# Kernel tuning notes

Measured on AMD Instinct MI355X. Metric: run time of the kernel, lower is better.

The kernel has to match this reference:

```python
import jax, jax.numpy as jnp
import numpy as np

N_NODES = 100000
N_EDGES = 1200000
D = 64
BN_EPS = 1e-5


def setup_inputs() -> dict:
    key = jax.random.key(0)
    ks = jax.random.split(key, 6)
    x = jax.random.normal(ks[0], (N_NODES, D), dtype=jnp.float32)
    edge_index = jax.random.randint(ks[1], (2, N_EDGES), 0, N_NODES, dtype=jnp.int64)
    # Linear params (Kaiming-uniform style scale)
    lim = 1.0 / np.sqrt(D)
    W = jax.random.uniform(ks[2], (D, D), dtype=jnp.float32, minval=-lim, maxval=lim)
    b = jax.random.uniform(ks[3], (D,), dtype=jnp.float32, minval=-lim, maxval=lim)
    gamma = jnp.ones((D,), dtype=jnp.float32)
    beta = jnp.zeros((D,), dtype=jnp.float32)
    C = jax.random.normal(ks[4], (D, D), dtype=jnp.float32) * 0.1
    return {"x": x, "edge_index": edge_index, "W": W, "b": b,
            "gamma": gamma, "beta": beta, "C": C}


def reference(x, edge_index, W, b, gamma, beta, C):
    n = x.shape[0]
    src, dst = edge_index[0], edge_index[1]
    # SimpleConv(aggr='mean', combine_root='sum'): mean over incoming messages + root
    msg_sum = jax.ops.segment_sum(x[src], dst, num_segments=n)            # [N, D]
    deg = jax.ops.segment_sum(jnp.ones_like(src, dtype=x.dtype), dst, num_segments=n)
    agg = msg_sum / jnp.maximum(deg, 1.0)[:, None]
    h = x + agg
    # Linear
    h = h @ W.T + b
    # BatchNorm1d (training mode: batch stats, biased variance)
    mean = jnp.mean(h, axis=0)
    var = jnp.mean((h - mean) ** 2, axis=0)
    h = (h - mean) * jax.lax.rsqrt(var + BN_EPS) * gamma + beta
    # AsymSwiGLU gate
    gate = jax.nn.sigmoid(h @ C)
    return gate * h
```

## Files before the change

kernel.cpp:

```cpp
#include <hip/hip_runtime.h>
#include <math.h>

#define D 64
#define BN_EPS 1e-5f

#define NBITS 7
#define BINSZ 128
#define MAXBINS 800
#define CAP 2048
#define CHUNK 4096
#define BUCKET 48
#define OP 68
#define WP 72

typedef short bf16x8 __attribute__((ext_vector_type(8)));
typedef float f32x4 __attribute__((ext_vector_type(4)));

__device__ __forceinline__ unsigned f2bf(float f) {
    unsigned u = __float_as_uint(f);
    return (u + 0x7FFFu + ((u >> 16) & 1u)) >> 16;
}
__device__ __forceinline__ float bf2f(unsigned short h) {
    return __uint_as_float(((unsigned)h) << 16);
}
__device__ __forceinline__ bf16x8 cvt8f(const float* __restrict__ p) {
    float4 a = ((const float4*)p)[0];
    float4 b = ((const float4*)p)[1];
    bf16x8 r;
    r[0] = (short)f2bf(a.x); r[1] = (short)f2bf(a.y);
    r[2] = (short)f2bf(a.z); r[3] = (short)f2bf(a.w);
    r[4] = (short)f2bf(b.x); r[5] = (short)f2bf(b.y);
    r[6] = (short)f2bf(b.z); r[7] = (short)f2bf(b.w);
    return r;
}

__global__ __launch_bounds__(256) void zero_kernel(int4* __restrict__ p, int n4) {
    int t = blockIdx.x * 256 + threadIdx.x;
    if (t < n4) p[t] = make_int4(0, 0, 0, 0);
}

__global__ __launch_bounds__(256) void xhalf_kernel(
    const float* __restrict__ x, unsigned short* __restrict__ xh, long long n8) {
    long long t = (long long)blockIdx.x * 256 + threadIdx.x;
    if (t >= n8) return;
    const float4* rp = (const float4*)(x + t * 8);
    float4 a = rp[0], b = rp[1];
    uint4 o;
    o.x = f2bf(a.x) | (f2bf(a.y) << 16);
    o.y = f2bf(a.z) | (f2bf(a.w) << 16);
    o.z = f2bf(b.x) | (f2bf(b.y) << 16);
    o.w = f2bf(b.z) | (f2bf(b.w) << 16);
    *(uint4*)(xh + t * 8) = o;
}

__global__ __launch_bounds__(1024) void binA_kernel(
    const int* __restrict__ ei, int* __restrict__ binCursor,
    unsigned* __restrict__ binBuf, int E, int nbins) {
    __shared__ unsigned short pos[CHUNK];
    __shared__ int hist[MAXBINS];
    __shared__ int base[MAXBINS];
    int tid = threadIdx.x;
    int c0 = blockIdx.x * CHUNK;

    for (int i = tid; i < nbins; i += 1024) hist[i] = 0;
    __syncthreads();

#pragma unroll
    for (int k = 0; k < CHUNK / 1024; ++k) {
        int i = k * 1024 + tid;
        int e = c0 + i;
        if (e < E) {
            int dst = ei[E + e];
            pos[i] = (unsigned short)atomicAdd(&hist[dst >> NBITS], 1);
        }
    }
    __syncthreads();

    for (int b = tid; b < nbins; b += 1024) {
        int h = hist[b];
        base[b] = h > 0 ? atomicAdd(&binCursor[b * 16], h) : 0;
    }
    __syncthreads();

#pragma unroll
    for (int k = 0; k < CHUNK / 1024; ++k) {
        int i = k * 1024 + tid;
        int e = c0 + i;
        if (e < E) {
            int src = ei[e];
            int dst = ei[E + e];
            int b = dst >> NBITS;
            int idx = base[b] + (int)pos[i];
            if (idx < CAP)
                binBuf[(size_t)b * CAP + idx] =
                    ((unsigned)src << NBITS) | (unsigned)(dst & (BINSZ - 1));
        }
    }
}

__global__ __launch_bounds__(256) void binSort_kernel(
    const unsigned* __restrict__ binBuf, const int* __restrict__ binCursor,
    int* __restrict__ csr, int* __restrict__ cnt, int N) {
    __shared__ int hist[BINSZ];
    int bin = blockIdx.x, tid = threadIdx.x;
    int nodeBase = bin << NBITS;
    int nrows = N - nodeBase; if (nrows > BINSZ) nrows = BINSZ;
    if (tid < BINSZ) hist[tid] = 0;
    __syncthreads();
    int nE = binCursor[bin * 16]; if (nE > CAP) nE = CAP;
    const unsigned* eb = binBuf + (size_t)bin * CAP;
    for (int i = tid; i < nE; i += 256) {
        unsigned r = eb[i];
        int dl = (int)(r & (BINSZ - 1));
        int src = (int)(r >> NBITS);
        int p = atomicAdd(&hist[dl], 1);
        if (p < BUCKET) csr[(size_t)(nodeBase + dl) * BUCKET + p] = src;
    }
    __syncthreads();
    for (int r = tid; r < nrows; r += 256) cnt[nodeBase + r] = hist[r];
}

__global__ __launch_bounds__(1024) void fusedGL_kernel(
    const unsigned short* __restrict__ xh, const int* __restrict__ csr,
    const int* __restrict__ cnt, const float* __restrict__ W,
    const float* __restrict__ bias, float* __restrict__ h,
    float* __restrict__ partial, int N) {
    __shared__ float tile[64 * OP];
    __shared__ unsigned short wt[64 * WP];
    __shared__ float psum[16 * 32];
    int tid = threadIdx.x;
    int lane = tid & 63;
    int w = tid >> 6;
    int rbase = blockIdx.x << 6;
    int nrows = N - rbase; if (nrows > 64) nrows = 64;

    {
        int r = tid >> 4, q = tid & 15;
        float4 v = *(const float4*)(W + (size_t)r * D + q * 4);
        uint2 o;
        o.x = f2bf(v.x) | (f2bf(v.y) << 16);
        o.y = f2bf(v.z) | (f2bf(v.w) << 16);
        *(uint2*)(wt + r * WP + q * 4) = o;
    }

    int c = lane & 15, g = lane >> 4;
    for (int i = 0; i < 4; ++i) {
        int nl = w * 4 + i;
        int node = rbase + nl;
        if (node < N) {
            int deg = cnt[node];
            deg = __builtin_amdgcn_readfirstlane(deg);
            int trips = deg < BUCKET ? deg : BUCKET;
            int sidx = lane < BUCKET ? csr[(size_t)node * BUCKET + lane] : 0;
            float a0 = 0.f, a1 = 0.f, a2 = 0.f, a3 = 0.f;
            if (trips > 0) {
                int nq = (trips + 3) >> 2;
                int last = trips - 1;
                uint2 v[12];
#pragma unroll
                for (int q = 0; q < 12; ++q) {
                    if (q < nq) {
                        int r = 4 * q + g;
                        int rc = r < trips ? r : last;
                        int s = __shfl(sidx, rc);
                        v[q] = *(const uint2*)(xh + (size_t)s * D + c * 4);
                    }
                }
#pragma unroll
                for (int q = 0; q < 12; ++q) {
                    if (q < nq) {
                        int r = 4 * q + g;
                        if (r < trips) {
                            unsigned lo = v[q].x, hi = v[q].y;
                            a0 += __uint_as_float(lo << 16);
                            a1 += __uint_as_float(lo & 0xFFFF0000u);
                            a2 += __uint_as_float(hi << 16);
                            a3 += __uint_as_float(hi & 0xFFFF0000u);
                        }
                    }
                }
            }
            a0 += __shfl_xor(a0, 16); a0 += __shfl_xor(a0, 32);
            a1 += __shfl_xor(a1, 16); a1 += __shfl_xor(a1, 32);
            a2 += __shfl_xor(a2, 16); a2 += __shfl_xor(a2, 32);
            a3 += __shfl_xor(a3, 16); a3 += __shfl_xor(a3, 32);
            float invd = deg > 0 ? 1.0f / (float)deg : 1.0f;
            if (g == 0) {
                uint2 rt = *(const uint2*)(xh + (size_t)node * D + c * 4);
                float4 o;
                o.x = __uint_as_float(rt.x << 16)         + a0 * invd;
                o.y = __uint_as_float(rt.x & 0xFFFF0000u) + a1 * invd;
                o.z = __uint_as_float(rt.y << 16)         + a2 * invd;
                o.w = __uint_as_float(rt.y & 0xFFFF0000u) + a3 * invd;
                *(float4*)(tile + nl * OP + c * 4) = o;
            }
        } else {
            if (g == 0)
                *(float4*)(tile + nl * OP + c * 4) = make_float4(0.f, 0.f, 0.f, 0.f);
        }
    }
    __syncthreads();

    int rb = w & 3, t = w >> 2;
    int ar = lane & 15, gg = lane >> 4;
    const float* arow = tile + (rb * 16 + ar) * OP + 8 * gg;
    bf16x8 A0 = cvt8f(arow);
    bf16x8 A1 = cvt8f(arow + 32);
    bf16x8 B0 = *(const bf16x8*)(wt + (t * 16 + ar) * WP + 8 * gg);
    bf16x8 B1 = *(const bf16x8*)(wt + (t * 16 + ar) * WP + 32 + 8 * gg);
    float bj = bias[t * 16 + ar];
    f32x4 acc;
    acc[0] = bj; acc[1] = bj; acc[2] = bj; acc[3] = bj;
    acc = __builtin_amdgcn_mfma_f32_16x16x32_bf16(A0, B0, acc, 0, 0, 0);
    acc = __builtin_amdgcn_mfma_f32_16x16x32_bf16(A1, B1, acc, 0, 0, 0);
    __syncthreads();

#pragma unroll
    for (int r = 0; r < 4; ++r)
        tile[(rb * 16 + 4 * gg + r) * OP + t * 16 + ar] = acc[r];
    float s = 0.f, q = 0.f;
#pragma unroll
    for (int r = 0; r < 4; ++r) {
        int row = rb * 16 + 4 * gg + r;
        float v = (row < nrows) ? acc[r] : 0.f;
        s += v; q += v * v;
    }
    s += __shfl_xor(s, 16); s += __shfl_xor(s, 32);
    q += __shfl_xor(q, 16); q += __shfl_xor(q, 32);
    if (lane < 16) {
        psum[w * 32 + lane] = s;
        psum[w * 32 + 16 + lane] = q;
    }
    __syncthreads();

    {
        int r = tid >> 4, cq = tid & 15;
        if (r < nrows)
            *(float4*)(h + (size_t)(rbase + r) * D + cq * 4) =
                *(const float4*)(tile + r * OP + cq * 4);
    }
    if (tid < 128) {
        int f = tid & 63;
        int off = (tid >= 64) ? 16 : 0;
        int t2 = f >> 4, col = f & 15;
        float a = 0.f;
#pragma unroll
        for (int rb2 = 0; rb2 < 4; ++rb2)
            a += psum[(t2 * 4 + rb2) * 32 + off + col];
        partial[(size_t)blockIdx.x * 128 + tid] = a;
    }
}

__global__ __launch_bounds__(256) void reduceBN_kernel(
    const float* __restrict__ partial, const float* __restrict__ gamma,
    const float* __restrict__ beta, float* __restrict__ ss,
    int nWG, float inv_n) {
    __shared__ float rs[256], rq[256];
    int f = blockIdx.x;
    int tid = threadIdx.x;
    float s = 0.f, q = 0.f;
    for (int w = tid; w < nWG; w += 256) {
        s += partial[(size_t)w * 128 + f];
        q += partial[(size_t)w * 128 + 64 + f];
    }
    rs[tid] = s; rq[tid] = q;
    __syncthreads();
    for (int st = 128; st > 0; st >>= 1) {
        if (tid < st) { rs[tid] += rs[tid + st]; rq[tid] += rq[tid + st]; }
        __syncthreads();
    }
    if (tid == 0) {
        float mean = rs[0] * inv_n;
        float var = rq[0] * inv_n - mean * mean;
        float rstd = rsqrtf(var + BN_EPS);
        float sc = gamma[f] * rstd;
        ss[f] = sc;
        ss[64 + f] = beta[f] - mean * sc;
    }
}

__global__ __launch_bounds__(256) void gateMFMA_kernel(
    float* __restrict__ h, const float* __restrict__ ss,
    const float* __restrict__ C, int N) {
    __shared__ float tile[64 * OP];
    __shared__ unsigned short ct[64 * WP];
    int tid = threadIdx.x;
    int lane = tid & 63;
    int w = tid >> 6;
    int ar = lane & 15, g = lane >> 4;
    int rbase = blockIdx.x << 6;
    int nrows = N - rbase; if (nrows > 64) nrows = 64;

#pragma unroll
    for (int it = 0; it < 4; ++it) {
        int u = it * 256 + tid;
        int r = u >> 4, c = u & 15;
        float4 v = (r < nrows)
            ? *(const float4*)(h + (size_t)(rbase + r) * D + c * 4)
            : make_float4(0.f, 0.f, 0.f, 0.f);
        *(float4*)(tile + r * OP + c * 4) = v;
    }
    {
        int k = tid >> 2, q = tid & 3;
        const float* cp = C + (size_t)k * D + q * 16;
#pragma unroll
        for (int i = 0; i < 16; ++i)
            ct[(q * 16 + i) * WP + k] = (unsigned short)f2bf(cp[i]);
    }
    __syncthreads();

    bool valid = (rbase + w * 16) < N;
    f32x4 acc[4];
    if (valid) {
        const float* arow = tile + (w * 16 + ar) * OP + 8 * g;
        float4 s0 = *(const float4*)(ss + 8 * g);
        float4 s1 = *(const float4*)(ss + 8 * g + 4);
        float4 o0 = *(const float4*)(ss + 64 + 8 * g);
        float4 o1 = *(const float4*)(ss + 64 + 8 * g + 4);
        float4 v0 = ((const float4*)arow)[0];
        float4 v1 = ((const float4*)arow)[1];
        bf16x8 a0, a1;
        a0[0] = (short)f2bf(v0.x * s0.x + o0.x);
        a0[1] = (short)f2bf(v0.y * s0.y + o0.y);
        a0[2] = (short)f2bf(v0.z * s0.z + o0.z);
        a0[3] = (short)f2bf(v0.w * s0.w + o0.w);
        a0[4] = (short)f2bf(v1.x * s1.x + o1.x);
        a0[5] = (short)f2bf(v1.y * s1.y + o1.y);
        a0[6] = (short)f2bf(v1.z * s1.z + o1.z);
        a0[7] = (short)f2bf(v1.w * s1.w + o1.w);
        float4 t0 = *(const float4*)(ss + 32 + 8 * g);
        float4 t1 = *(const float4*)(ss + 32 + 8 * g + 4);
        float4 u0 = *(const float4*)(ss + 96 + 8 * g);
        float4 u1 = *(const float4*)(ss + 96 + 8 * g + 4);
        float4 w0 = ((const float4*)(arow + 32))[0];
        float4 w1 = ((const float4*)(arow + 32))[1];
        a1[0] = (short)f2bf(w0.x * t0.x + u0.x);
        a1[1] = (short)f2bf(w0.y * t0.y + u0.y);
        a1[2] = (short)f2bf(w0.z * t0.z + u0.z);
        a1[3] = (short)f2bf(w0.w * t0.w + u0.w);
        a1[4] = (short)f2bf(w1.x * t1.x + u1.x);
        a1[5] = (short)f2bf(w1.y * t1.y + u1.y);
        a1[6] = (short)f2bf(w1.z * t1.z + u1.z);
        a1[7] = (short)f2bf(w1.w * t1.w + u1.w);
#pragma unroll
        for (int t = 0; t < 4; ++t) {
            bf16x8 b0 = *(const bf16x8*)(ct + (t * 16 + ar) * WP + 8 * g);
            bf16x8 b1 = *(const bf16x8*)(ct + (t * 16 + ar) * WP + 32 + 8 * g);
            acc[t][0] = 0.f; acc[t][1] = 0.f; acc[t][2] = 0.f; acc[t][3] = 0.f;
            acc[t] = __builtin_amdgcn_mfma_f32_16x16x32_bf16(a0, b0, acc[t], 0, 0, 0);
            acc[t] = __builtin_amdgcn_mfma_f32_16x16x32_bf16(a1, b1, acc[t], 0, 0, 0);
        }
#pragma unroll
        for (int t = 0; t < 4; ++t) {
            float scC = ss[t * 16 + ar];
            float shC = ss[64 + t * 16 + ar];
#pragma unroll
            for (int r = 0; r < 4; ++r) {
                int idx = (w * 16 + 4 * g + r) * OP + t * 16 + ar;
                float hn = tile[idx] * scC + shC;
                float gg = 1.0f / (1.0f + __expf(-acc[t][r]));
                tile[idx] = gg * hn;
            }
        }
    }
    __syncthreads();

#pragma unroll
    for (int it = 0; it < 4; ++it) {
        int u = it * 256 + tid;
        int r = u >> 4, c = u & 15;
        if (r < nrows)
            *(float4*)(h + (size_t)(rbase + r) * D + c * 4) =
                *(const float4*)(tile + r * OP + c * 4);
    }
}

extern "C" void kernel_launch(void* const* d_in, const int* in_sizes, int n_in,
                              void* d_out, int out_size, void* d_ws, size_t ws_size,
                              hipStream_t stream) {
    const float* x     = (const float*)d_in[0];
    const int*   ei    = (const int*)d_in[1];
    const float* W     = (const float*)d_in[2];
    const float* b     = (const float*)d_in[3];
    const float* gamma = (const float*)d_in[4];
    const float* beta  = (const float*)d_in[5];
    const float* C     = (const float*)d_in[6];
    float* out = (float*)d_out;

    const int N = in_sizes[0] / D;
    const int E = in_sizes[1] / 2;
    const int nbins = (N + BINSZ - 1) >> NBITS;
    const int nWGlin = (N + 63) / 64;

    int*            binCursor = (int*)d_ws;
    float*          ss        = (float*)(binCursor + (size_t)nbins * 16);
    int*            cnt       = (int*)(ss + 128);
    int*            csr       = cnt + N;
    unsigned*       binBuf    = (unsigned*)(csr + (size_t)N * BUCKET);
    float*          partial   = (float*)(binBuf + (size_t)nbins * CAP);
    unsigned short* xh        = (unsigned short*)(partial + (size_t)nWGlin * 128);

    {
        int n4 = (nbins * 16 + 128) / 4;
        zero_kernel<<<(n4 + 255) / 256, 256, 0, stream>>>((int4*)d_ws, n4);
    }
    {
        long long n8 = (long long)N * D / 8;
        xhalf_kernel<<<(int)((n8 + 255) / 256), 256, 0, stream>>>(x, xh, n8);
    }
    binA_kernel<<<(E + CHUNK - 1) / CHUNK, 1024, 0, stream>>>(ei, binCursor, binBuf, E, nbins);
    binSort_kernel<<<nbins, 256, 0, stream>>>(binBuf, binCursor, csr, cnt, N);
    fusedGL_kernel<<<nWGlin, 1024, 0, stream>>>(xh, csr, cnt, W, b, out, partial, N);
    reduceBN_kernel<<<64, 256, 0, stream>>>(partial, gamma, beta, ss, nWGlin, 1.0f / (float)N);
    gateMFMA_kernel<<<(N + 63) / 64, 256, 0, stream>>>(out, ss, C, N);
}
```

Before: 117.4 us.

## Fuse bin sort into gather-linear kernel with LDS-resident per-node CSR

Removes the separate binSort kernel and its global CSR and count arrays. Each gather-linear workgroup now scans its half of a 128-node bin from binBuf and builds a 64-node bucketed adjacency list and degree histogram in shared memory, aliased onto the output tile buffer. This drops a kernel launch and a large global write and read of the padded CSR, at the cost of every bin being scanned twice, once by each half-workgroup. It also writes the aggregated tile directly as bf16 into a separate LDS buffer, which removes the fp32-to-bf16 conversion at the MFMA operand load and one barrier.

```diff
diff --git a/kernel.cpp b/kernel.cpp
--- a/kernel.cpp
+++ b/kernel.cpp
@@ -22,16 +22,6 @@
 }
 __device__ __forceinline__ float bf2f(unsigned short h) {
     return __uint_as_float(((unsigned)h) << 16);
-}
-__device__ __forceinline__ bf16x8 cvt8f(const float* __restrict__ p) {
-    float4 a = ((const float4*)p)[0];
-    float4 b = ((const float4*)p)[1];
-    bf16x8 r;
-    r[0] = (short)f2bf(a.x); r[1] = (short)f2bf(a.y);
-    r[2] = (short)f2bf(a.z); r[3] = (short)f2bf(a.w);
-    r[4] = (short)f2bf(b.x); r[5] = (short)f2bf(b.y);
-    r[6] = (short)f2bf(b.z); r[7] = (short)f2bf(b.w);
-    return r;
 }
 
 __global__ __launch_bounds__(256) void zero_kernel(int4* __restrict__ p, int n4) {
@@ -98,40 +88,23 @@
     }
 }
 
-__global__ __launch_bounds__(256) void binSort_kernel(
-    const unsigned* __restrict__ binBuf, const int* __restrict__ binCursor,
-    int* __restrict__ csr, int* __restrict__ cnt, int N) {
-    __shared__ int hist[BINSZ];
-    int bin = blockIdx.x, tid = threadIdx.x;
-    int nodeBase = bin << NBITS;
-    int nrows = N - nodeBase; if (nrows > BINSZ) nrows = BINSZ;
-    if (tid < BINSZ) hist[tid] = 0;
-    __syncthreads();
-    int nE = binCursor[bin * 16]; if (nE > CAP) nE = CAP;
-    const unsigned* eb = binBuf + (size_t)bin * CAP;
-    for (int i = tid; i < nE; i += 256) {
-        unsigned r = eb[i];
-        int dl = (int)(r & (BINSZ - 1));
-        int src = (int)(r >> NBITS);
-        int p = atomicAdd(&hist[dl], 1);
-        if (p < BUCKET) csr[(size_t)(nodeBase + dl) * BUCKET + p] = src;
-    }
-    __syncthreads();
-    for (int r = tid; r < nrows; r += 256) cnt[nodeBase + r] = hist[r];
-}
-
-__global__ __launch_bounds__(1024) void fusedGL_kernel(
-    const unsigned short* __restrict__ xh, const int* __restrict__ csr,
-    const int* __restrict__ cnt, const float* __restrict__ W,
+__global__ __launch_bounds__(1024) void fusedGLS_kernel(
+    const unsigned short* __restrict__ xh, const unsigned* __restrict__ binBuf,
+    const int* __restrict__ binCursor, const float* __restrict__ W,
     const float* __restrict__ bias, float* __restrict__ h,
     float* __restrict__ partial, int N) {
-    __shared__ float tile[64 * OP];
     __shared__ unsigned short wt[64 * WP];
+    __shared__ unsigned short ta[64 * WP];
+    __shared__ float uni[64 * OP];
+    __shared__ int hist[64];
     __shared__ float psum[16 * 32];
+    int* lcsr = (int*)uni;
+
     int tid = threadIdx.x;
     int lane = tid & 63;
     int w = tid >> 6;
     int rbase = blockIdx.x << 6;
+    int bin = blockIdx.x >> 1, half = blockIdx.x & 1;
     int nrows = N - rbase; if (nrows > 64) nrows = 64;
 
     {
@@ -142,16 +115,33 @@
         o.y = f2bf(v.z) | (f2bf(v.w) << 16);
         *(uint2*)(wt + r * WP + q * 4) = o;
     }
+    if (tid < 64) hist[tid] = 0;
+    __syncthreads();
+
+    {
+        int nE = binCursor[bin * 16]; if (nE > CAP) nE = CAP;
+        const unsigned* eb = binBuf + (size_t)bin * CAP;
+        for (int i = tid; i < nE; i += 1024) {
+            unsigned r = eb[i];
+            int dl = (int)(r & (BINSZ - 1));
+            if ((dl >> 6) == half) {
+                int d2 = dl & 63;
+                int p = atomicAdd(&hist[d2], 1);
+                if (p < BUCKET) lcsr[d2 * BUCKET + p] = (int)(r >> NBITS);
+            }
+        }
+    }
+    __syncthreads();
 
     int c = lane & 15, g = lane >> 4;
     for (int i = 0; i < 4; ++i) {
         int nl = w * 4 + i;
         int node = rbase + nl;
         if (node < N) {
-            int deg = cnt[node];
+            int deg = hist[nl];
             deg = __builtin_amdgcn_readfirstlane(deg);
             int trips = deg < BUCKET ? deg : BUCKET;
-            int sidx = lane < BUCKET ? csr[(size_t)node * BUCKET + lane] : 0;
+            int sidx = lane < BUCKET ? lcsr[nl * BUCKET + lane] : 0;
             float a0 = 0.f, a1 = 0.f, a2 = 0.f, a3 = 0.f;
             if (trips > 0) {
                 int nq = (trips + 3) >> 2;
@@ -187,25 +177,25 @@
             float invd = deg > 0 ? 1.0f / (float)deg : 1.0f;
             if (g == 0) {
                 uint2 rt = *(const uint2*)(xh + (size_t)node * D + c * 4);
-                float4 o;
-                o.x = __uint_as_float(rt.x << 16)         + a0 * invd;
-                o.y = __uint_as_float(rt.x & 0xFFFF0000u) + a1 * invd;
-                o.z = __uint_as_float(rt.y << 16)         + a2 * invd;
-                o.w = __uint_as_float(rt.y & 0xFFFF0000u) + a3 * invd;
-                *(float4*)(tile + nl * OP + c * 4) = o;
+                float f0 = __uint_as_float(rt.x << 16)         + a0 * invd;
+                float f1 = __uint_as_float(rt.x & 0xFFFF0000u) + a1 * invd;
+                float f2 = __uint_as_float(rt.y << 16)         + a2 * invd;
+                float f3 = __uint_as_float(rt.y & 0xFFFF0000u) + a3 * invd;
+                uint2 o;
+                o.x = f2bf(f0) | (f2bf(f1) << 16);
+                o.y = f2bf(f2) | (f2bf(f3) << 16);
+                *(uint2*)(ta + nl * WP + c * 4) = o;
             }
-        } else {
-            if (g == 0)
-                *(float4*)(tile + nl * OP + c * 4) = make_float4(0.f, 0.f, 0.f, 0.f);
+        } else if (g == 0) {
+            *(uint2*)(ta + nl * WP + c * 4) = make_uint2(0u, 0u);
         }
     }
     __syncthreads();
 
     int rb = w & 3, t = w >> 2;
     int ar = lane & 15, gg = lane >> 4;
-    const float* arow = tile + (rb * 16 + ar) * OP + 8 * gg;
-    bf16x8 A0 = cvt8f(arow);
-    bf16x8 A1 = cvt8f(arow + 32);
+    bf16x8 A0 = *(const bf16x8*)(ta + (rb * 16 + ar) * WP + 8 * gg);
+    bf16x8 A1 = *(const bf16x8*)(ta + (rb * 16 + ar) * WP + 32 + 8 * gg);
     bf16x8 B0 = *(const bf16x8*)(wt + (t * 16 + ar) * WP + 8 * gg);
     bf16x8 B1 = *(const bf16x8*)(wt + (t * 16 + ar) * WP + 32 + 8 * gg);
     float bj = bias[t * 16 + ar];
@@ -213,11 +203,10 @@
     acc[0] = bj; acc[1] = bj; acc[2] = bj; acc[3] = bj;
     acc = __builtin_amdgcn_mfma_f32_16x16x32_bf16(A0, B0, acc, 0, 0, 0);
     acc = __builtin_amdgcn_mfma_f32_16x16x32_bf16(A1, B1, acc, 0, 0, 0);
-    __syncthreads();
 
 #pragma unroll
     for (int r = 0; r < 4; ++r)
-        tile[(rb * 16 + 4 * gg + r) * OP + t * 16 + ar] = acc[r];
+        uni[(rb * 16 + 4 * gg + r) * OP + t * 16 + ar] = acc[r];
     float s = 0.f, q = 0.f;
 #pragma unroll
     for (int r = 0; r < 4; ++r) {
@@ -237,7 +226,7 @@
         int r = tid >> 4, cq = tid & 15;
         if (r < nrows)
             *(float4*)(h + (size_t)(rbase + r) * D + cq * 4) =
-                *(const float4*)(tile + r * OP + cq * 4);
+                *(const float4*)(uni + r * OP + cq * 4);
     }
     if (tid < 128) {
         int f = tid & 63;
@@ -394,9 +383,7 @@
 
     int*            binCursor = (int*)d_ws;
     float*          ss        = (float*)(binCursor + (size_t)nbins * 16);
-    int*            cnt       = (int*)(ss + 128);
-    int*            csr       = cnt + N;
-    unsigned*       binBuf    = (unsigned*)(csr + (size_t)N * BUCKET);
+    unsigned*       binBuf    = (unsigned*)(ss + 128);
     float*          partial   = (float*)(binBuf + (size_t)nbins * CAP);
     unsigned short* xh        = (unsigned short*)(partial + (size_t)nWGlin * 128);
 
@@ -409,8 +396,7 @@
         xhalf_kernel<<<(int)((n8 + 255) / 256), 256, 0, stream>>>(x, xh, n8);
     }
     binA_kernel<<<(E + CHUNK - 1) / CHUNK, 1024, 0, stream>>>(ei, binCursor, binBuf, E, nbins);
-    binSort_kernel<<<nbins, 256, 0, stream>>>(binBuf, binCursor, csr, cnt, N);
-    fusedGL_kernel<<<nWGlin, 1024, 0, stream>>>(xh, csr, cnt, W, b, out, partial, N);
+    fusedGLS_kernel<<<nWGlin, 1024, 0, stream>>>(xh, binBuf, binCursor, W, b, out, partial, N);
     reduceBN_kernel<<<64, 256, 0, stream>>>(partial, gamma, beta, ss, nWGlin, 1.0f / (float)N);
     gateMFMA_kernel<<<(N + 63) / 64, 256, 0, stream>>>(out, ss, C, N);
 }
```

Result: faster. 108.7 us (-7.4%).
